# Optimization experiments

Measured on AMD Instinct MI355X. Metric: run time of the kernel, lower is better.

## Reference

```python
import jax, jax.numpy as jnp
import numpy as np

N = 100000       # nodes
E = 1000000      # edges
IN = 128         # in_dim
HID = 64         # hid_dim
NET = 4          # n_etypes
STEPS = 5        # n_steps
G = 128          # graphs in batch
LBL = 10         # num_labels


def setup_inputs() -> dict:
    key = jax.random.key(0)
    ks = jax.random.split(key, 20)
    def w(k, shape, fan_in):
        return jax.random.normal(k, shape, jnp.float32) / np.sqrt(fan_in)
    return dict(
        x=jax.random.normal(ks[0], (N, IN), jnp.float32),
        src=jax.random.randint(ks[1], (E,), 0, N),
        dst=jax.random.randint(ks[2], (E,), 0, N),
        etype=jax.random.randint(ks[3], (E,), 0, NET),
        node2graph=jnp.sort(jax.random.randint(ks[4], (N,), 0, G)),
        # linear_in
        W_in=w(ks[5], (HID, IN), IN), b_in=jnp.zeros((HID,), jnp.float32),
        # per-edge-type linears [n_etypes, out, in]
        We=w(ks[6], (NET, HID, HID), HID), be=jnp.zeros((NET, HID), jnp.float32),
        # GRUCell (torch layout: rows = [r; z; n])
        W_ih=w(ks[7], (3 * HID, HID), HID), b_ih=jnp.zeros((3 * HID,), jnp.float32),
        W_hh=w(ks[8], (3 * HID, HID), HID), b_hh=jnp.zeros((3 * HID,), jnp.float32),
        # classifier
        W1=w(ks[9], (HID // 2, HID), HID), b1=jnp.zeros((HID // 2,), jnp.float32),
        W2=w(ks[10], (LBL, HID // 2), HID // 2), b2=jnp.zeros((LBL,), jnp.float32),
    )


def reference(x, W_in, b_in, We, be, W_ih, b_ih, W_hh, b_hh, W1, b1, W2, b2,
              src, dst, etype, node2graph):
    h = x @ W_in.T + b_in                                  # [N, HID]
    for _ in range(STEPS):
        # per-etype linear on node states: trans[e] = h @ We[e].T + be[e]
        trans = jnp.einsum('nd,efd->enf', h, We) + be[:, None, :]  # [NET, N, HID]
        msgs = trans[etype, src]                           # [E, HID] gather per edge
        a = jax.ops.segment_sum(msgs, dst, num_segments=N)  # scatter-add aggregation
        # GRUCell(a, h)
        gi = a @ W_ih.T + b_ih
        gh = h @ W_hh.T + b_hh
        ir, iz, i_n = jnp.split(gi, 3, axis=-1)
        hr, hz, h_n = jnp.split(gh, 3, axis=-1)
        r = jax.nn.sigmoid(ir + hr)
        z = jax.nn.sigmoid(iz + hz)
        n = jnp.tanh(i_n + r * h_n)
        h = (1.0 - z) * n + z * h
    # dgl.mean_nodes: per-graph mean of node states
    cnt = jnp.maximum(jax.ops.segment_sum(jnp.ones((N,), h.dtype), node2graph, num_segments=G), 1.0)
    hg = jax.ops.segment_sum(h, node2graph, num_segments=G) / cnt[:, None]  # [G, HID]
    return jax.nn.relu(hg @ W1.T + b1) @ W2.T + b2         # [G, LBL]
```

## Files before the change

### kernel.cpp

```cpp
#include <hip/hip_runtime.h>
#include <hip/hip_bf16.h>
#include <math.h>

#define N_NODES 100000
#define N_EDGES 1000000
#define IN_DIM 128
#define HID 64
#define NET 4
#define STEPS 5
#define G_GRAPHS 128
#define LBL 10
#define NGRP 6250
#define NBKT 1024
#define TILE_E 8192

typedef __attribute__((ext_vector_type(8))) short short8;
typedef __attribute__((ext_vector_type(4))) float f32x4;
typedef unsigned short ushort_t;

__device__ inline ushort_t f2bf(float v) {
    __hip_bfloat16 b = __float2bfloat16(v);
    return __builtin_bit_cast(ushort_t, b);
}
__device__ inline float bf2f(ushort_t u) {
    __hip_bfloat16 b = __builtin_bit_cast(__hip_bfloat16, u);
    return __bfloat162float(b);
}


__global__ void k_pack_bc(const float* __restrict__ We, ushort_t* __restrict__ BC) {
    int idx = blockIdx.x * blockDim.x + threadIdx.x;
    if (idx >= 24 * 4 * 64 * 8) return;
    int j = idx & 7, lane = (idx >> 3) & 63, ct = (idx >> 9) & 3, sl = idx >> 11;
    int g = lane >> 4, u = lane & 15;
    int p = sl >> 3, ks = sl & 7;
    int k = ks * 32 + g * 8 + j;
    int t = k >> 6, d = k & 63;
    int o = ct * 16 + u;
    float val = We[t * 4096 + o * 64 + d];
    ushort_t hi = f2bf(val);
    BC[idx] = (p < 2) ? hi : f2bf(val - bf2f(hi));
}

__global__ void k_pack_b2(const float* __restrict__ W_ih, const float* __restrict__ b_ih,
                          const float* __restrict__ W_hh, const float* __restrict__ b_hh,
                          ushort_t* __restrict__ B2, float* __restrict__ bg2) {
    int idx = blockIdx.x * blockDim.x + threadIdx.x;
    if (idx >= 12 * 16 * 4 * 16 * 8) return;
    int j = idx & 7, u = (idx >> 3) & 15, g = (idx >> 7) & 3, ct = (idx >> 9) & 15, s = idx >> 13;
    int m = ct * 16 + u;
    int q = m >> 6, gate = (m >> 4) & 3, c = q * 16 + (m & 15);
    int k = (s & 3) * 32 + g * 8 + j;
    float val;
    if (gate == 0)      { int jr = c;        val = (k < 64) ? W_ih[jr * 64 + k] : W_hh[jr * 64 + k - 64]; }
    else if (gate == 1) { int jr = 64 + c;   val = (k < 64) ? W_ih[jr * 64 + k] : W_hh[jr * 64 + k - 64]; }
    else if (gate == 2) { int jr = 128 + c;  val = (k < 64) ? W_ih[jr * 64 + k] : 0.f; }
    else                { int jr = 128 + c;  val = (k < 64) ? 0.f : W_hh[jr * 64 + k - 64]; }
    ushort_t hi = f2bf(val);
    B2[idx] = (s < 8) ? hi : f2bf(val - bf2f(hi));
    if (s == 0 && g == 0 && j == 0) {
        float bv;
        if (gate == 0)      bv = b_ih[c] + b_hh[c];
        else if (gate == 1) bv = b_ih[64 + c] + b_hh[64 + c];
        else if (gate == 2) bv = b_ih[128 + c];
        else                bv = b_hh[128 + c];
        bg2[m] = bv;
    }
}

__global__ void k_pack_bin(const float* __restrict__ W_in, ushort_t* __restrict__ BIN) {
    int idx = blockIdx.x * blockDim.x + threadIdx.x;
    if (idx >= 24576) return;
    int j = idx & 7, lu = (idx >> 3) & 63, ct = (idx >> 9) & 3, s = idx >> 11;
    int g = lu >> 4, u = lu & 15;
    int m = ct * 16 + u;
    int k = (s & 3) * 32 + g * 8 + j;
    float val = W_in[m * 128 + k];
    ushort_t hi = f2bf(val);
    BIN[idx] = (s < 8) ? hi : f2bf(val - bf2f(hi));
}

__global__ __launch_bounds__(256) void k_linear_in(const float* __restrict__ x,
        const ushort_t* __restrict__ BIN, const float* __restrict__ b_in,
        ushort_t* __restrict__ AH, ushort_t* __restrict__ hrow) {
    __shared__ float hlds[4][16 * 68];
    int tid = threadIdx.x;
    int lane = tid & 63, wp = tid >> 6;
    int g = lane >> 4, u = lane & 15;
    int grp = blockIdx.x * 4 + wp;
    bool ok = grp < NGRP;
    int row = ok ? (grp * 16 + u) : 0;
    short8 xhi[4], xlo[4];
    #pragma unroll
    for (int ks = 0; ks < 4; ++ks) {
        const float* xp = &x[(size_t)row * 128 + ks * 32 + g * 8];
        float4 v0 = ok ? *(const float4*)xp : make_float4(0.f, 0.f, 0.f, 0.f);
        float4 v1 = ok ? *(const float4*)(xp + 4) : make_float4(0.f, 0.f, 0.f, 0.f);
        float vv[8] = {v0.x, v0.y, v0.z, v0.w, v1.x, v1.y, v1.z, v1.w};
        #pragma unroll
        for (int j = 0; j < 8; ++j) {
            ushort_t hh = f2bf(vv[j]);
            xhi[ks][j] = (short)hh;
            xlo[ks][j] = (short)f2bf(vv[j] - bf2f(hh));
        }
    }
    f32x4 zero = {0.f, 0.f, 0.f, 0.f};
    f32x4 acc[4] = {zero, zero, zero, zero};
    #pragma unroll
    for (int s = 0; s < 12; ++s) {
        int ks = s & 3;
        short8 af = (s < 4) ? xhi[ks] : (s < 8) ? xlo[ks] : xhi[ks];
        #pragma unroll
        for (int ct = 0; ct < 4; ++ct) {
            short8 bf = *(const short8*)&BIN[((size_t)(s * 4 + ct) * 64 + lane) * 8];
            acc[ct] = __builtin_amdgcn_mfma_f32_16x16x32_bf16(af, bf, acc[ct], 0, 0, 0);
        }
    }
    #pragma unroll
    for (int ct = 0; ct < 4; ++ct) {
        float bo = b_in[ct * 16 + u];
        #pragma unroll
        for (int j = 0; j < 4; ++j)
            hlds[wp][(g * 4 + j) * 68 + ct * 16 + u] = acc[ct][j] + bo;
    }
    __syncthreads();
    #pragma unroll
    for (int k = 0; k < 4; ++k) {
        int bi = g + 4 * k;
        short8 ov;
        #pragma unroll
        for (int j = 0; j < 8; ++j) {
            float v = hlds[wp][u * 68 + (bi & 7) * 8 + j];
            ushort_t hh = f2bf(v);
            ov[j] = (bi < 8) ? (short)hh : (short)f2bf(v - bf2f(hh));
        }
        int blk = (bi < 8) ? (8 + bi) : (24 + (bi - 8));
        if (ok) {
            *(short8*)&AH[((size_t)grp * 32 + blk) * 128 + u * 8] = ov;
            if (bi < 8)
                *(short8*)&hrow[((size_t)(grp * 16 + u)) * 64 + bi * 8] = ov;
        }
    }
}

__global__ __launch_bounds__(256) void k_bhist(const int* __restrict__ dst,
        int* __restrict__ bhist) {
    __shared__ int h[NBKT];
    for (int i = threadIdx.x; i < NBKT; i += 256) h[i] = 0;
    __syncthreads();
    int idx = blockIdx.x * 256 + threadIdx.x;
    for (int e = idx; e < N_EDGES; e += 256 * 256) atomicAdd(&h[dst[e] >> 7], 1);
    __syncthreads();
    for (int i = threadIdx.x; i < NBKT; i += 256) {
        int c = h[i];
        if (c) atomicAdd(&bhist[i], c);
    }
}

__global__ __launch_bounds__(1024) void k_bscan(const int* __restrict__ bhist,
        int* __restrict__ bbase, int* __restrict__ bcursor) {
    __shared__ int ts[NBKT];
    int t = threadIdx.x;
    int v = bhist[t];
    ts[t] = v;
    __syncthreads();
    for (int off = 1; off < NBKT; off <<= 1) {
        int u = (t >= off) ? ts[t - off] : 0;
        __syncthreads();
        ts[t] += u;
        __syncthreads();
    }
    int excl = ts[t] - v;
    bbase[t] = excl;
    bcursor[t] = excl;
    if (t == NBKT - 1) bbase[NBKT] = ts[NBKT - 1];
}

__global__ __launch_bounds__(512) void k_bscatter(const int* __restrict__ src,
        const int* __restrict__ dst, const int* __restrict__ et,
        int* __restrict__ bcursor, unsigned int* __restrict__ ebuf) {
    __shared__ int hcnt[NBKT], loff[NBKT], gpos[NBKT], ps[512];
    __shared__ unsigned int stage[TILE_E];
    __shared__ unsigned short sbkt[TILE_E];
    int tid = threadIdx.x;
    int base = blockIdx.x * TILE_E;
    int tilecnt = min(TILE_E, N_EDGES - base);
    for (int i = tid; i < NBKT; i += 512) hcnt[i] = 0;
    __syncthreads();
    #pragma unroll
    for (int k = 0; k < TILE_E / 512; ++k) {
        int e = base + tid + k * 512;
        if (e < N_EDGES) atomicAdd(&hcnt[dst[e] >> 7], 1);
    }
    __syncthreads();
    int c0 = hcnt[tid * 2], c1 = hcnt[tid * 2 + 1];
    ps[tid] = c0 + c1;
    __syncthreads();
    for (int off = 1; off < 512; off <<= 1) {
        int u = (tid >= off) ? ps[tid - off] : 0;
        __syncthreads();
        ps[tid] += u;
        __syncthreads();
    }
    int ex = ps[tid] - (c0 + c1);
    loff[tid * 2] = ex;
    loff[tid * 2 + 1] = ex + c0;
    for (int b = tid; b < NBKT; b += 512) {
        int c = hcnt[b];
        gpos[b] = c ? atomicAdd(&bcursor[b], c) : 0;
    }
    __syncthreads();
    for (int i = tid; i < NBKT; i += 512) hcnt[i] = 0;
    __syncthreads();
    #pragma unroll
    for (int k = 0; k < TILE_E / 512; ++k) {
        int e = base + tid + k * 512;
        if (e < N_EDGES) {
            int d = dst[e];
            int b = d >> 7;
            int r = atomicAdd(&hcnt[b], 1);
            int lp = loff[b] + r;
            stage[lp] = (unsigned int)src[e] | ((unsigned int)et[e] << 20)
                      | ((unsigned int)(d & 127) << 22);
            sbkt[lp] = (unsigned short)b;
        }
    }
    __syncthreads();
    for (int i = tid; i < tilecnt; i += 512) {
        int b = sbkt[i];
        ebuf[gpos[b] + (i - loff[b])] = stage[i];
    }
}

__global__ __launch_bounds__(256) void k_bcsr(const unsigned int* __restrict__ ebuf,
        const int* __restrict__ bbase, int* __restrict__ adj, int* __restrict__ row_ptr2) {
    __shared__ int ncnt[512], noff[513], ps[256];
    int b = blockIdx.x;
    int tid = threadIdx.x;
    int ebeg = bbase[b], eend = bbase[b + 1];
    int ecnt = eend - ebeg;
    ncnt[tid] = 0; ncnt[tid + 256] = 0;
    __syncthreads();
    for (int i = tid; i < ecnt; i += 256) {
        unsigned int p = ebuf[ebeg + i];
        int key = (int)((((p >> 22) & 127) << 2) | ((p >> 20) & 3));
        atomicAdd(&ncnt[key], 1);
    }
    __syncthreads();
    int c0 = ncnt[2 * tid], c1 = ncnt[2 * tid + 1];
    ps[tid] = c0 + c1;
    __syncthreads();
    for (int off = 1; off < 256; off <<= 1) {
        int u = (tid >= off) ? ps[tid - off] : 0;
        __syncthreads();
        ps[tid] += u;
        __syncthreads();
    }
    int ex = ps[tid] - (c0 + c1);
    noff[2 * tid] = ex;
    noff[2 * tid + 1] = ex + c0;
    if (tid == 255) noff[512] = ps[255];
    __syncthreads();
    ncnt[tid] = 0; ncnt[tid + 256] = 0;
    __syncthreads();
    for (int i = tid; i < ecnt; i += 256) {
        unsigned int p = ebuf[ebeg + i];
        int key = (int)((((p >> 22) & 127) << 2) | ((p >> 20) & 3));
        int r = atomicAdd(&ncnt[key], 1);
        adj[ebeg + noff[key] + r] = (int)(p & 0xFFFFF);
    }
    for (int k = tid; k < 512; k += 256)
        row_ptr2[b * 512 + k] = ebeg + noff[k];
    if (b == NBKT - 1 && tid == 0) row_ptr2[NBKT * 512] = eend;
}

__global__ __launch_bounds__(512) void k_step(const int* __restrict__ row_ptr2,
        const int* __restrict__ adj, const ushort_t* __restrict__ hin,
        ushort_t* __restrict__ hout, ushort_t* __restrict__ AH,
        const ushort_t* __restrict__ BC, const float* __restrict__ be,
        const ushort_t* __restrict__ B2, const float* __restrict__ bg2) {
    __shared__ float smem[8448];
    float* aggf = smem;
    float* cnts = smem + 8320;
    ushort_t* als  = (ushort_t*)smem;
    ushort_t* hlds = (ushort_t*)((char*)smem + 9216);

    int tid = threadIdx.x, lane = tid & 63, wp = tid >> 6;
    int g = lane >> 4, u = lane & 15;
    int grp0 = blockIdx.x * 2;
    int nbase = grp0 * 16;

    #pragma unroll 1
    for (int r = 0; r < 4; ++r) {
        int nl = wp * 4 + r;
        int n = nbase + nl;
        const int* op = &row_ptr2[(size_t)n * 4];
        int o0 = op[0], o1 = op[1], o2 = op[2], o3 = op[3], o4 = op[4];
        #pragma unroll
        for (int t = 0; t < 4; ++t) {
            int i = (t == 0) ? o0 : (t == 1) ? o1 : (t == 2) ? o2 : o3;
            int e = (t == 0) ? o1 : (t == 1) ? o2 : (t == 2) ? o3 : o4;
            float s0 = 0.f, s1 = 0.f, s2 = 0.f, s3 = 0.f;
            for (; i + 4 <= e; i += 4) {
                int a0 = adj[i], a1 = adj[i + 1], a2 = adj[i + 2], a3 = adj[i + 3];
                s0 += bf2f(hin[(size_t)a0 * 64 + lane]);
                s1 += bf2f(hin[(size_t)a1 * 64 + lane]);
                s2 += bf2f(hin[(size_t)a2 * 64 + lane]);
                s3 += bf2f(hin[(size_t)a3 * 64 + lane]);
            }
            for (; i < e; ++i)
                s0 += bf2f(hin[(size_t)adj[i] * 64 + lane]);
            aggf[nl * 260 + t * 64 + lane] = (s0 + s1) + (s2 + s3);
        }
        if (lane == 0) {
            cnts[nl * 4 + 0] = (float)(o1 - o0);
            cnts[nl * 4 + 1] = (float)(o2 - o1);
            cnts[nl * 4 + 2] = (float)(o3 - o2);
            cnts[nl * 4 + 3] = (float)(o4 - o3);
        }
    }
    __syncthreads();

    int rp1 = wp >> 2, cq = wp & 3;
    f32x4 zero = {0.f, 0.f, 0.f, 0.f};
    f32x4 acc1 = zero;
    #pragma unroll
    for (int ks = 0; ks < 8; ++ks) {
        const float* ap = &aggf[(rp1 * 16 + u) * 260 + ks * 32 + g * 8];
        f32x4 x0 = *(const f32x4*)ap;
        f32x4 x1 = *(const f32x4*)(ap + 4);
        short8 ahi, alo;
        #pragma unroll
        for (int j = 0; j < 4; ++j) {
            ushort_t hh = f2bf(x0[j]);
            ahi[j] = (short)hh; alo[j] = (short)f2bf(x0[j] - bf2f(hh));
            ushort_t hh2 = f2bf(x1[j]);
            ahi[4 + j] = (short)hh2; alo[4 + j] = (short)f2bf(x1[j] - bf2f(hh2));
        }
        #pragma unroll
        for (int p = 0; p < 3; ++p) {
            short8 af = (p == 1) ? alo : ahi;
            short8 bf = *(const short8*)&BC[((size_t)((p * 8 + ks) * 4 + cq) * 64 + lane) * 8];
            acc1 = __builtin_amdgcn_mfma_f32_16x16x32_bf16(af, bf, acc1, 0, 0, 0);
        }
    }
    __syncthreads();

    {
        float beL[4];
        #pragma unroll
        for (int t = 0; t < 4; ++t) beL[t] = be[t * 64 + cq * 16 + u];
        #pragma unroll
        for (int j = 0; j < 4; ++j) {
            int row = rp1 * 16 + g * 4 + j;
            f32x4 cn = *(const f32x4*)&cnts[row * 4];
            float v = acc1[j] + cn[0] * beL[0] + cn[1] * beL[1]
                              + cn[2] * beL[2] + cn[3] * beL[3];
            int col = cq * 16 + u;
            ushort_t hh = f2bf(v);
            als[row * 136 + col] = hh;
            als[row * 136 + 64 + col] = f2bf(v - bf2f(hh));
        }
    }
    {
        int c = tid;
        int gl = c >> 8, rr = c & 255, bi = rr >> 4, uu = rr & 15;
        int blk = (bi < 8) ? (8 + bi) : (24 + (bi - 8));
        *(short8*)&hlds[((gl * 16 + bi) * 16 + uu) * 8] =
            *(const short8*)&AH[((size_t)(grp0 + gl) * 32 + blk) * 128 + uu * 8];
    }
    __syncthreads();

    int q = wp & 3, rp2 = wp >> 2;
    f32x4 acc2[4] = {zero, zero, zero, zero};
    #pragma unroll
    for (int s = 0; s < 12; ++s) {
        int p2 = s >> 2, ks2 = s & 3;
        short8 afr;
        if (ks2 < 2) {
            int base = ((p2 == 1) ? 64 : 0) + ks2 * 32 + g * 8;
            afr = *(const short8*)&als[(rp2 * 16 + u) * 136 + base];
        } else {
            int part = (p2 == 1) ? 1 : 0;
            int bi = part * 8 + (ks2 - 2) * 4 + g;
            afr = *(const short8*)&hlds[((rp2 * 16 + bi) * 16 + u) * 8];
        }
        #pragma unroll
        for (int ct = 0; ct < 4; ++ct) {
            short8 bfr = *(const short8*)&B2[((size_t)(s * 16 + q * 4 + ct) * 64 + g * 16 + u) * 8];
            acc2[ct] = __builtin_amdgcn_mfma_f32_16x16x32_bf16(afr, bfr, acc2[ct], 0, 0, 0);
        }
    }
    __syncthreads();

    {
        float bgv[4];
        #pragma unroll
        for (int ct = 0; ct < 4; ++ct) bgv[ct] = bg2[q * 64 + ct * 16 + u];
        int hid = q * 16 + u;
        #pragma unroll
        for (int j = 0; j < 4; ++j) {
            int uu = g * 4 + j;
            int shi = ((rp2 * 16 + (hid >> 3)) * 16 + uu) * 8 + (hid & 7);
            int slo = ((rp2 * 16 + 8 + (hid >> 3)) * 16 + uu) * 8 + (hid & 7);
            float ho = bf2f(hlds[shi]) + bf2f(hlds[slo]);
            float rs  = acc2[0][j] + bgv[0];
            float zs  = acc2[1][j] + bgv[1];
            float inn = acc2[2][j] + bgv[2];
            float hnn = acc2[3][j] + bgv[3];
            float rr = 1.f / (1.f + __expf(-rs));
            float zz = 1.f / (1.f + __expf(-zs));
            float t = inn + rr * hnn;
            float e2 = __expf(2.f * t);
            float nn = 1.f - 2.f / (e2 + 1.f);
            float hnew = (1.f - zz) * nn + zz * ho;
            ushort_t hh = f2bf(hnew);
            hlds[shi] = hh;
            hlds[slo] = f2bf(hnew - bf2f(hh));
        }
    }
    __syncthreads();

    {
        int c = tid;
        int gl = c >> 8, rr = c & 255, bi = rr >> 4, uu = rr & 15;
        short8 v = *(const short8*)&hlds[((gl * 16 + bi) * 16 + uu) * 8];
        int blk = (bi < 8) ? (8 + bi) : (24 + (bi - 8));
        *(short8*)&AH[((size_t)(grp0 + gl) * 32 + blk) * 128 + uu * 8] = v;
        if (bi < 8)
            *(short8*)&hout[((size_t)((grp0 + gl) * 16 + uu)) * 64 + bi * 8] = v;
    }
}

__global__ __launch_bounds__(256) void k_pool(const int* __restrict__ n2g,
        const ushort_t* __restrict__ AH, float* __restrict__ hg) {
    int gidx = blockIdx.x;
    int lo = 0, hi = N_NODES;
    while (lo < hi) { int mid = (lo + hi) >> 1; if (n2g[mid] < gidx) lo = mid + 1; else hi = mid; }
    int s = lo;
    hi = N_NODES;
    while (lo < hi) { int mid = (lo + hi) >> 1; if (n2g[mid] < gidx + 1) lo = mid + 1; else hi = mid; }
    int e = lo;
    int w = threadIdx.x >> 6, lane = threadIdx.x & 63;
    int bh = 8 + (lane >> 3), bl = 24 + (lane >> 3), el = lane & 7;
    float sum = 0.f;
    for (int n = s + w; n < e; n += 4) {
        size_t base = (size_t)(n >> 4) * 4096 + (size_t)(n & 15) * 8;
        sum += bf2f(AH[base + bh * 128 + el]) + bf2f(AH[base + bl * 128 + el]);
    }
    __shared__ float red[4][64];
    red[w][lane] = sum;
    __syncthreads();
    if (threadIdx.x < 64) {
        float tot = red[0][lane] + red[1][lane] + red[2][lane] + red[3][lane];
        float cnt = (float)(e - s);
        hg[gidx * 64 + lane] = tot / fmaxf(cnt, 1.f);
    }
}

__global__ __launch_bounds__(64) void k_cls(const float* __restrict__ hg,
        const float* __restrict__ W1, const float* __restrict__ b1,
        const float* __restrict__ W2, const float* __restrict__ b2,
        float* __restrict__ out) {
    int gidx = blockIdx.x;
    __shared__ float v[64];
    __shared__ float m[32];
    v[threadIdx.x] = hg[gidx * 64 + threadIdx.x];
    __syncthreads();
    if (threadIdx.x < 32) {
        float a = b1[threadIdx.x];
        #pragma unroll 8
        for (int k = 0; k < 64; ++k) a = fmaf(v[k], W1[threadIdx.x * 64 + k], a);
        m[threadIdx.x] = fmaxf(a, 0.f);
    }
    __syncthreads();
    if (threadIdx.x < 10) {
        float a = b2[threadIdx.x];
        #pragma unroll
        for (int j = 0; j < 32; ++j) a = fmaf(m[j], W2[threadIdx.x * 32 + j], a);
        out[gidx * 10 + threadIdx.x] = a;
    }
}

extern "C" void kernel_launch(void* const* d_in, const int* in_sizes, int n_in,
                              void* d_out, int out_size, void* d_ws, size_t ws_size,
                              hipStream_t stream) {
    const float* x    = (const float*)d_in[0];
    const int* src    = (const int*)d_in[1];
    const int* dst    = (const int*)d_in[2];
    const int* etype  = (const int*)d_in[3];
    const int* n2g    = (const int*)d_in[4];
    const float* W_in = (const float*)d_in[5];
    const float* b_in = (const float*)d_in[6];
    const float* We   = (const float*)d_in[7];
    const float* be   = (const float*)d_in[8];
    const float* W_ih = (const float*)d_in[9];
    const float* b_ih = (const float*)d_in[10];
    const float* W_hh = (const float*)d_in[11];
    const float* b_hh = (const float*)d_in[12];
    const float* W1   = (const float*)d_in[13];
    const float* b1   = (const float*)d_in[14];
    const float* W2   = (const float*)d_in[15];
    const float* b2   = (const float*)d_in[16];
    float* out = (float*)d_out;

    char* wsb = (char*)d_ws;
    size_t off = 0;
    auto alloc = [&](size_t bytes) -> void* {
        void* p = wsb + off;
        off += (bytes + 255) & ~(size_t)255;
        return p;
    };
    ushort_t* AH       = (ushort_t*)alloc((size_t)NGRP * 4096 * 2);
    ushort_t* hrowA    = (ushort_t*)alloc((size_t)N_NODES * 64 * 2);
    ushort_t* hrowB    = (ushort_t*)alloc((size_t)N_NODES * 64 * 2);
    int*      adj      = (int*)     alloc((size_t)N_EDGES * 4);
    unsigned int* ebuf = (unsigned int*)alloc((size_t)N_EDGES * 4);
    int*      row_ptr2 = (int*)     alloc(((size_t)NBKT * 512 + 1) * 4);
    int*      bhist    = (int*)     alloc((size_t)NBKT * 4);
    int*      bbase    = (int*)     alloc((size_t)(NBKT + 1) * 4);
    int*      bcursor  = (int*)     alloc((size_t)NBKT * 4);
    ushort_t* B2       = (ushort_t*)alloc((size_t)12 * 16 * 4 * 16 * 8 * 2);
    float*    bg2      = (float*)   alloc(256 * 4);
    ushort_t* BIN      = (ushort_t*)alloc((size_t)24576 * 2);
    ushort_t* BC       = (ushort_t*)alloc((size_t)24 * 4 * 64 * 8 * 2);
    float*    hg       = (float*)   alloc(128 * 64 * 4);

    hipLaunchKernelGGL(k_pack_b2, dim3(384), dim3(256), 0, stream, W_ih, b_ih, W_hh, b_hh, B2, bg2);
    hipLaunchKernelGGL(k_pack_bin, dim3(96), dim3(256), 0, stream, W_in, BIN);
    hipLaunchKernelGGL(k_pack_bc, dim3(192), dim3(256), 0, stream, We, BC);
    hipLaunchKernelGGL(k_linear_in, dim3((NGRP + 3) / 4), dim3(256), 0, stream, x, BIN, b_in, AH, hrowA);

    hipMemsetAsync(bhist, 0, (size_t)NBKT * 4, stream);
    hipLaunchKernelGGL(k_bhist, dim3(256), dim3(256), 0, stream, dst, bhist);
    hipLaunchKernelGGL(k_bscan, dim3(1), dim3(1024), 0, stream, bhist, bbase, bcursor);
    hipLaunchKernelGGL(k_bscatter, dim3((N_EDGES + TILE_E - 1) / TILE_E), dim3(512), 0, stream,
                       src, dst, etype, bcursor, ebuf);
    hipLaunchKernelGGL(k_bcsr, dim3(NBKT), dim3(256), 0, stream, ebuf, bbase, adj, row_ptr2);

    int sblk = NGRP / 2;
    for (int step = 0; step < STEPS; ++step) {
        const ushort_t* hin = (step & 1) ? hrowB : hrowA;
        ushort_t* hout      = (step & 1) ? hrowA : hrowB;
        hipLaunchKernelGGL(k_step, dim3(sblk), dim3(512), 0, stream,
                           row_ptr2, adj, hin, hout, AH, BC, be, B2, bg2);
    }
    hipLaunchKernelGGL(k_pool, dim3(G_GRAPHS), dim3(256), 0, stream, n2g, AH, hg);
    hipLaunchKernelGGL(k_cls, dim3(G_GRAPHS), dim3(64), 0, stream, hg, W1, b1, W2, b2, out);
}
```

Baseline: 825.6 us.

## Interleave per-node edge gathers and replace tiled AH state with row-major hi/lo buffers

The gather loop in the step kernel now walks all 8 (node, etype) edge lists of two nodes at once, with predicated lanes. This keeps eight independent gathers in flight instead of four within one list, and it drops the per-list remainder loop. The MFMA-tiled AH state buffer is removed. The hidden state's high and low bf16 parts are now kept in separate row-major, double-buffered arrays, which also feed the pooling kernel. This cuts the duplicate write of the high part to both AH and hrow each step. The cost is wasted lanes when list lengths differ, and more registers in the gather loop.

After: 816.7 us. Within noise of the previous version (-1.1%).

```diff
diff --git a/kernel.cpp b/kernel.cpp
--- a/kernel.cpp
+++ b/kernel.cpp
@@ -82,7 +82,7 @@
 
 __global__ __launch_bounds__(256) void k_linear_in(const float* __restrict__ x,
         const ushort_t* __restrict__ BIN, const float* __restrict__ b_in,
-        ushort_t* __restrict__ AH, ushort_t* __restrict__ hrow) {
+        ushort_t* __restrict__ hrow, ushort_t* __restrict__ lrow) {
     __shared__ float hlds[4][16 * 68];
     int tid = threadIdx.x;
     int lane = tid & 63, wp = tid >> 6;
@@ -134,11 +134,10 @@
             ushort_t hh = f2bf(v);
             ov[j] = (bi < 8) ? (short)hh : (short)f2bf(v - bf2f(hh));
         }
-        int blk = (bi < 8) ? (8 + bi) : (24 + (bi - 8));
         if (ok) {
-            *(short8*)&AH[((size_t)grp * 32 + blk) * 128 + u * 8] = ov;
-            if (bi < 8)
-                *(short8*)&hrow[((size_t)(grp * 16 + u)) * 64 + bi * 8] = ov;
+            size_t base = (size_t)(grp * 16 + u) * 64;
+            if (bi < 8) *(short8*)&hrow[base + bi * 8] = ov;
+            else        *(short8*)&lrow[base + (bi - 8) * 8] = ov;
         }
     }
 }
@@ -276,7 +275,8 @@
 
 __global__ __launch_bounds__(512) void k_step(const int* __restrict__ row_ptr2,
         const int* __restrict__ adj, const ushort_t* __restrict__ hin,
-        ushort_t* __restrict__ hout, ushort_t* __restrict__ AH,
+        const ushort_t* __restrict__ lin, ushort_t* __restrict__ hout,
+        ushort_t* __restrict__ lout,
         const ushort_t* __restrict__ BC, const float* __restrict__ be,
         const ushort_t* __restrict__ B2, const float* __restrict__ bg2) {
     __shared__ float smem[8448];
@@ -291,32 +291,62 @@
     int nbase = grp0 * 16;
 
     #pragma unroll 1
-    for (int r = 0; r < 4; ++r) {
-        int nl = wp * 4 + r;
-        int n = nbase + nl;
-        const int* op = &row_ptr2[(size_t)n * 4];
-        int o0 = op[0], o1 = op[1], o2 = op[2], o3 = op[3], o4 = op[4];
-        #pragma unroll
-        for (int t = 0; t < 4; ++t) {
-            int i = (t == 0) ? o0 : (t == 1) ? o1 : (t == 2) ? o2 : o3;
-            int e = (t == 0) ? o1 : (t == 1) ? o2 : (t == 2) ? o3 : o4;
-            float s0 = 0.f, s1 = 0.f, s2 = 0.f, s3 = 0.f;
-            for (; i + 4 <= e; i += 4) {
-                int a0 = adj[i], a1 = adj[i + 1], a2 = adj[i + 2], a3 = adj[i + 3];
-                s0 += bf2f(hin[(size_t)a0 * 64 + lane]);
-                s1 += bf2f(hin[(size_t)a1 * 64 + lane]);
-                s2 += bf2f(hin[(size_t)a2 * 64 + lane]);
-                s3 += bf2f(hin[(size_t)a3 * 64 + lane]);
-            }
-            for (; i < e; ++i)
-                s0 += bf2f(hin[(size_t)adj[i] * 64 + lane]);
-            aggf[nl * 260 + t * 64 + lane] = (s0 + s1) + (s2 + s3);
-        }
+    for (int pr = 0; pr < 2; ++pr) {
+        int nl0 = wp * 4 + pr * 2;
+        const int* op = &row_ptr2[(size_t)(nbase + nl0) * 4];
+        int b0 = op[0], b1 = op[1], b2 = op[2], b3 = op[3], b4 = op[4];
+        int b5 = op[5], b6 = op[6], b7 = op[7], b8 = op[8];
+        int i0 = b0, i1 = b1, i2 = b2, i3 = b3, i4 = b4, i5 = b5, i6 = b6, i7 = b7;
+        float s0 = 0.f, s1 = 0.f, s2 = 0.f, s3 = 0.f, s4 = 0.f, s5 = 0.f, s6 = 0.f, s7 = 0.f;
+        bool c0 = i0 < b1, c1 = i1 < b2, c2 = i2 < b3, c3 = i3 < b4;
+        bool c4 = i4 < b5, c5 = i5 < b6, c6 = i6 < b7, c7 = i7 < b8;
+        int a0 = adj[c0 ? i0 : 0], a1 = adj[c1 ? i1 : 0];
+        int a2 = adj[c2 ? i2 : 0], a3 = adj[c3 ? i3 : 0];
+        int a4 = adj[c4 ? i4 : 0], a5 = adj[c5 ? i5 : 0];
+        int a6 = adj[c6 ? i6 : 0], a7 = adj[c7 ? i7 : 0];
+        while (c0 | c1 | c2 | c3 | c4 | c5 | c6 | c7) {
+            ushort_t w0 = hin[(size_t)a0 * 64 + lane];
+            ushort_t w1 = hin[(size_t)a1 * 64 + lane];
+            ushort_t w2 = hin[(size_t)a2 * 64 + lane];
+            ushort_t w3 = hin[(size_t)a3 * 64 + lane];
+            ushort_t w4 = hin[(size_t)a4 * 64 + lane];
+            ushort_t w5 = hin[(size_t)a5 * 64 + lane];
+            ushort_t w6 = hin[(size_t)a6 * 64 + lane];
+            ushort_t w7 = hin[(size_t)a7 * 64 + lane];
+            i0 += c0; i1 += c1; i2 += c2; i3 += c3;
+            i4 += c4; i5 += c5; i6 += c6; i7 += c7;
+            s0 += c0 ? bf2f(w0) : 0.f;
+            s1 += c1 ? bf2f(w1) : 0.f;
+            s2 += c2 ? bf2f(w2) : 0.f;
+            s3 += c3 ? bf2f(w3) : 0.f;
+            s4 += c4 ? bf2f(w4) : 0.f;
+            s5 += c5 ? bf2f(w5) : 0.f;
+            s6 += c6 ? bf2f(w6) : 0.f;
+            s7 += c7 ? bf2f(w7) : 0.f;
+            c0 = i0 < b1; c1 = i1 < b2; c2 = i2 < b3; c3 = i3 < b4;
+            c4 = i4 < b5; c5 = i5 < b6; c6 = i6 < b7; c7 = i7 < b8;
+            a0 = adj[c0 ? i0 : 0]; a1 = adj[c1 ? i1 : 0];
+            a2 = adj[c2 ? i2 : 0]; a3 = adj[c3 ? i3 : 0];
+            a4 = adj[c4 ? i4 : 0]; a5 = adj[c5 ? i5 : 0];
+            a6 = adj[c6 ? i6 : 0]; a7 = adj[c7 ? i7 : 0];
+        }
+        aggf[nl0 * 260 +   0 + lane] = s0;
+        aggf[nl0 * 260 +  64 + lane] = s1;
+        aggf[nl0 * 260 + 128 + lane] = s2;
+        aggf[nl0 * 260 + 192 + lane] = s3;
+        aggf[(nl0 + 1) * 260 +   0 + lane] = s4;
+        aggf[(nl0 + 1) * 260 +  64 + lane] = s5;
+        aggf[(nl0 + 1) * 260 + 128 + lane] = s6;
+        aggf[(nl0 + 1) * 260 + 192 + lane] = s7;
         if (lane == 0) {
-            cnts[nl * 4 + 0] = (float)(o1 - o0);
-            cnts[nl * 4 + 1] = (float)(o2 - o1);
-            cnts[nl * 4 + 2] = (float)(o3 - o2);
-            cnts[nl * 4 + 3] = (float)(o4 - o3);
+            cnts[nl0 * 4 + 0] = (float)(b1 - b0);
+            cnts[nl0 * 4 + 1] = (float)(b2 - b1);
+            cnts[nl0 * 4 + 2] = (float)(b3 - b2);
+            cnts[nl0 * 4 + 3] = (float)(b4 - b3);
+            cnts[(nl0 + 1) * 4 + 0] = (float)(b5 - b4);
+            cnts[(nl0 + 1) * 4 + 1] = (float)(b6 - b5);
+            cnts[(nl0 + 1) * 4 + 2] = (float)(b7 - b6);
+            cnts[(nl0 + 1) * 4 + 3] = (float)(b8 - b7);
         }
     }
     __syncthreads();
@@ -365,9 +395,10 @@
     {
         int c = tid;
         int gl = c >> 8, rr = c & 255, bi = rr >> 4, uu = rr & 15;
-        int blk = (bi < 8) ? (8 + bi) : (24 + (bi - 8));
-        *(short8*)&hlds[((gl * 16 + bi) * 16 + uu) * 8] =
-            *(const short8*)&AH[((size_t)(grp0 + gl) * 32 + blk) * 128 + uu * 8];
+        size_t base = (size_t)(nbase + gl * 16 + uu) * 64;
+        short8 v = (bi < 8) ? *(const short8*)&hin[base + bi * 8]
+                            : *(const short8*)&lin[base + (bi - 8) * 8];
+        *(short8*)&hlds[((gl * 16 + bi) * 16 + uu) * 8] = v;
     }
     __syncthreads();
 
@@ -425,15 +456,15 @@
         int c = tid;
         int gl = c >> 8, rr = c & 255, bi = rr >> 4, uu = rr & 15;
         short8 v = *(const short8*)&hlds[((gl * 16 + bi) * 16 + uu) * 8];
-        int blk = (bi < 8) ? (8 + bi) : (24 + (bi - 8));
-        *(short8*)&AH[((size_t)(grp0 + gl) * 32 + blk) * 128 + uu * 8] = v;
-        if (bi < 8)
-            *(short8*)&hout[((size_t)((grp0 + gl) * 16 + uu)) * 64 + bi * 8] = v;
+        size_t base = (size_t)(nbase + gl * 16 + uu) * 64;
+        if (bi < 8) *(short8*)&hout[base + bi * 8] = v;
+        else        *(short8*)&lout[base + (bi - 8) * 8] = v;
     }
 }
 
 __global__ __launch_bounds__(256) void k_pool(const int* __restrict__ n2g,
-        const ushort_t* __restrict__ AH, float* __restrict__ hg) {
+        const ushort_t* __restrict__ hrow, const ushort_t* __restrict__ lrow,
+        float* __restrict__ hg) {
     int gidx = blockIdx.x;
     int lo = 0, hi = N_NODES;
     while (lo < hi) { int mid = (lo + hi) >> 1; if (n2g[mid] < gidx) lo = mid + 1; else hi = mid; }
@@ -442,12 +473,9 @@
     while (lo < hi) { int mid = (lo + hi) >> 1; if (n2g[mid] < gidx + 1) lo = mid + 1; else hi = mid; }
     int e = lo;
     int w = threadIdx.x >> 6, lane = threadIdx.x & 63;
-    int bh = 8 + (lane >> 3), bl = 24 + (lane >> 3), el = lane & 7;
     float sum = 0.f;
-    for (int n = s + w; n < e; n += 4) {
-        size_t base = (size_t)(n >> 4) * 4096 + (size_t)(n & 15) * 8;
-        sum += bf2f(AH[base + bh * 128 + el]) + bf2f(AH[base + bl * 128 + el]);
-    }
+    for (int n = s + w; n < e; n += 4)
+        sum += bf2f(hrow[(size_t)n * 64 + lane]) + bf2f(lrow[(size_t)n * 64 + lane]);
     __shared__ float red[4][64];
     red[w][lane] = sum;
     __syncthreads();
@@ -511,9 +539,10 @@
         off += (bytes + 255) & ~(size_t)255;
         return p;
     };
-    ushort_t* AH       = (ushort_t*)alloc((size_t)NGRP * 4096 * 2);
     ushort_t* hrowA    = (ushort_t*)alloc((size_t)N_NODES * 64 * 2);
+    ushort_t* lrowA    = (ushort_t*)alloc((size_t)N_NODES * 64 * 2);
     ushort_t* hrowB    = (ushort_t*)alloc((size_t)N_NODES * 64 * 2);
+    ushort_t* lrowB    = (ushort_t*)alloc((size_t)N_NODES * 64 * 2);
     int*      adj      = (int*)     alloc((size_t)N_EDGES * 4);
     unsigned int* ebuf = (unsigned int*)alloc((size_t)N_EDGES * 4);
     int*      row_ptr2 = (int*)     alloc(((size_t)NBKT * 512 + 1) * 4);
@@ -529,7 +558,7 @@
     hipLaunchKernelGGL(k_pack_b2, dim3(384), dim3(256), 0, stream, W_ih, b_ih, W_hh, b_hh, B2, bg2);
     hipLaunchKernelGGL(k_pack_bin, dim3(96), dim3(256), 0, stream, W_in, BIN);
     hipLaunchKernelGGL(k_pack_bc, dim3(192), dim3(256), 0, stream, We, BC);
-    hipLaunchKernelGGL(k_linear_in, dim3((NGRP + 3) / 4), dim3(256), 0, stream, x, BIN, b_in, AH, hrowA);
+    hipLaunchKernelGGL(k_linear_in, dim3((NGRP + 3) / 4), dim3(256), 0, stream, x, BIN, b_in, hrowA, lrowA);
 
     hipMemsetAsync(bhist, 0, (size_t)NBKT * 4, stream);
     hipLaunchKernelGGL(k_bhist, dim3(256), dim3(256), 0, stream, dst, bhist);
@@ -541,10 +570,12 @@
     int sblk = NGRP / 2;
     for (int step = 0; step < STEPS; ++step) {
         const ushort_t* hin = (step & 1) ? hrowB : hrowA;
+        const ushort_t* lin = (step & 1) ? lrowB : lrowA;
         ushort_t* hout      = (step & 1) ? hrowA : hrowB;
+        ushort_t* lout      = (step & 1) ? lrowA : lrowB;
         hipLaunchKernelGGL(k_step, dim3(sblk), dim3(512), 0, stream,
-                           row_ptr2, adj, hin, hout, AH, BC, be, B2, bg2);
-    }
-    hipLaunchKernelGGL(k_pool, dim3(G_GRAPHS), dim3(256), 0, stream, n2g, AH, hg);
+                           row_ptr2, adj, hin, lin, hout, lout, BC, be, B2, bg2);
+    }
+    hipLaunchKernelGGL(k_pool, dim3(G_GRAPHS), dim3(256), 0, stream, n2g, hrowB, lrowB, hg);
     hipLaunchKernelGGL(k_cls, dim3(G_GRAPHS), dim3(64), 0, stream, hg, W1, b1, W2, b2, out);
 }
```
